# Optimization experiments

Measured on AMD Instinct MI355X. Metric: run time of the kernel, lower is better.

The kernel has to match this reference:

```python
import jax, jax.numpy as jnp
import numpy as np

H = 51  # hidden size hardcoded in the module
B, T, FUT = 4096, 512, 16


def setup_inputs() -> dict:
    key = jax.random.key(0)
    ks = jax.random.split(key, 12)
    s = 1.0 / np.sqrt(H)  # PyTorch default uniform init bound
    u = lambda k, shape: jax.random.uniform(k, shape, jnp.float32, -s, s)
    return {
        "input": jax.random.normal(ks[0], (B, T), jnp.float32),
        "W_ih1": u(ks[1], (4 * H, 1)),
        "W_hh1": u(ks[2], (4 * H, H)),
        "b_ih1": u(ks[3], (4 * H,)),
        "b_hh1": u(ks[4], (4 * H,)),
        "W_ih2": u(ks[5], (4 * H, H)),
        "W_hh2": u(ks[6], (4 * H, H)),
        "b_ih2": u(ks[7], (4 * H,)),
        "b_hh2": u(ks[8], (4 * H,)),
        "W_lin": u(ks[9], (1, H)),
        "b_lin": u(ks[10], (1,)),
        "future": FUT,
    }


def _cell(x, h, c, Wih, Whh, b):
    # PyTorch LSTMCell gate order: i, f, g, o
    g = x @ Wih.T + h @ Whh.T + b
    i, f, gg, o = jnp.split(g, 4, axis=-1)
    c = jax.nn.sigmoid(f) * c + jax.nn.sigmoid(i) * jnp.tanh(gg)
    h = jax.nn.sigmoid(o) * jnp.tanh(c)
    return h, c


def _forward(input, W_ih1, W_hh1, b_ih1, b_hh1, W_ih2, W_hh2, b_ih2, b_hh2, W_lin, b_lin, future):
    bsz = input.shape[0]
    dt = input.dtype
    b1 = b_ih1 + b_hh1
    b2 = b_ih2 + b_hh2
    z = jnp.zeros((bsz, H), dt)
    init = (z, z, z, z)

    def step(carry, x_t):
        h1, c1, h2, c2 = carry
        h1, c1 = _cell(x_t[:, None], h1, c1, W_ih1, W_hh1, b1)
        h2, c2 = _cell(h1, h2, c2, W_ih2, W_hh2, b2)
        out = h2 @ W_lin.T + b_lin  # [b, 1]
        return (h1, c1, h2, c2), out

    (h1, c1, h2, c2), outs = jax.lax.scan(step, init, input.T)  # outs: [t, b, 1]

    def fstep(carry, _):
        h1, c1, h2, c2, out = carry
        h1, c1 = _cell(out, h1, c1, W_ih1, W_hh1, b1)
        h2, c2 = _cell(h1, h2, c2, W_ih2, W_hh2, b2)
        out = h2 @ W_lin.T + b_lin
        return (h1, c1, h2, c2, out), out

    _, fouts = jax.lax.scan(fstep, (h1, c1, h2, c2, outs[-1]), None, length=future)
    all_outs = jnp.concatenate([outs, fouts], axis=0)  # [t+future, b, 1]
    return all_outs[..., 0].T  # [b, t+future]


def reference(input, W_ih1, W_hh1, b_ih1, b_hh1, W_ih2, W_hh2, b_ih2, b_hh2, W_lin, b_lin, future):
    return _forward(input, W_ih1, W_hh1, b_ih1, b_hh1, W_ih2, W_hh2, b_ih2, b_hh2, W_lin, b_lin, future)
```

## Files before the change

kernel.cpp:

```cpp
#include <hip/hip_runtime.h>

#define TSEQ 512
#define FUT  16
#define OT   (TSEQ + FUT)
#define NB   16
#define NWAVE 13
#define NTHREADS (NWAVE * 64)
#define OBS  20

typedef _Float16 f16x8 __attribute__((ext_vector_type(8)));
typedef float    f32x4 __attribute__((ext_vector_type(4)));

#define NL2E  (-1.44269504089f)
#define N2L2E (-2.88539008178f)

__device__ __forceinline__ f32x4 mfma16(f16x8 a, f16x8 b, f32x4 c) {
    return __builtin_amdgcn_mfma_f32_16x16x32_f16(a, b, c, 0, 0, 0);
}

__device__ __forceinline__ float exp2fast(float x) {
#if __has_builtin(__builtin_amdgcn_exp2f)
    return __builtin_amdgcn_exp2f(x);
#else
    float r;
    asm("v_exp_f32 %0, %1\n\ts_nop 1" : "=v"(r) : "v"(x));
    return r;
#endif
}

__device__ __forceinline__ float cell2(const f32x4 acc, float& c) {
    const float Ei = exp2fast(acc[0]);
    const float Ef = exp2fast(acc[1]);
    const float Eg = exp2fast(acc[2]);
    const float Eo = exp2fast(acc[3]);
    const float sf   = __builtin_amdgcn_rcpf(1.0f + Ef);
    const float sitg = (1.0f - Eg) * __builtin_amdgcn_rcpf((1.0f + Ei) * (1.0f + Eg));
    c = fmaf(sf, c, sitg);
    const float Ec = exp2fast(c * N2L2E);
    return (1.0f - Ec) * __builtin_amdgcn_rcpf((1.0f + Eo) * (1.0f + Ec));
}

__global__ __launch_bounds__(NTHREADS, 1) void lstm_mfma_kernel(
    const float* __restrict__ input,
    const float* __restrict__ W_ih1,
    const float* __restrict__ W_hh1,
    const float* __restrict__ b_ih1,
    const float* __restrict__ b_hh1,
    const float* __restrict__ W_ih2,
    const float* __restrict__ W_hh2,
    const float* __restrict__ b_ih2,
    const float* __restrict__ b_hh2,
    const float* __restrict__ W_lin,
    const float* __restrict__ b_lin,
    float* __restrict__ out)
{
    const int tid  = threadIdx.x;
    const int w    = tid >> 6;
    const int lane = tid & 63;
    const int n    = lane & 15;
    const int q    = lane >> 4;
    const int b0   = blockIdx.x * NB;

    __shared__ _Float16 H1[2][2][64][8] __attribute__((aligned(16)));
    __shared__ _Float16 H2[2][2][64][8] __attribute__((aligned(16)));
    __shared__ float OB[2][16][OBS] __attribute__((aligned(16)));

    const int ru  = 4 * w + (n >> 2);
    const bool rv = (ru < 51);
    const int R   = 51 * (n & 3) + (rv ? ru : 50);
    const bool olin_row = (w == 12) && (n == 12);
    const float rsc = ((n & 3) == 2) ? N2L2E : NL2E;

    f16x8 W1h[2], W1l[2], W2h[4], W2l[4];
#pragma unroll
    for (int s = 0; s < 2; ++s) {
#pragma unroll
        for (int e = 0; e < 8; ++e) {
            const int k = 32 * s + 8 * q + e;
            float wv = 0.0f;
            if (rv) {
                if (k < 51)       wv = rsc * W_hh1[R * 51 + k];
                else if (k == 51) wv = rsc * W_ih1[R];
            }
            const _Float16 hi = (_Float16)wv;
            W1h[s][e] = hi;
            W1l[s][e] = (_Float16)(wv - (float)hi);
        }
    }
#pragma unroll
    for (int s = 0; s < 4; ++s) {
#pragma unroll
        for (int e = 0; e < 8; ++e) {
            const int k = 32 * s + 8 * q + e;
            float wv = 0.0f;
            if (rv) {
                if (k < 51)                  wv = rsc * W_ih2[R * 51 + k];
                else if (k >= 64 && k < 115) wv = rsc * W_hh2[R * 51 + (k - 64)];
            } else if (olin_row) {
                if (k >= 64 && k < 115)      wv = W_lin[k - 64];
            }
            const _Float16 hi = (_Float16)wv;
            W2h[s][e] = hi;
            W2l[s][e] = (_Float16)(wv - (float)hi);
        }
    }

    const int uu = 4 * w + q;
    const bool ustore = (uu < 51);
    const bool oduty = (w == 12) && (q == 3);
    f32x4 bias1v, bias2v;
#pragma unroll
    for (int r = 0; r < 4; ++r) {
        const int row = 51 * r + (ustore ? uu : 50);
        const float s = (r == 2) ? N2L2E : NL2E;
        bias1v[r] = ustore ? s * (b_ih1[row] + b_hh1[row]) : 0.0f;
        bias2v[r] = ustore ? s * (b_ih2[row] + b_hh2[row]) : 0.0f;
    }
    const float blin = b_lin[0];
    if (oduty) bias2v[0] = blin;
    const float wlin = ustore ? W_lin[uu] : 0.0f;
    const int uuX = ustore ? uu : 60;
    const int us = uuX >> 5;
    const int lp = n + 16 * ((uuX & 31) >> 3);
    const int ue = uuX & 7;

    {
        const f16x8 zz = {0, 0, 0, 0, 0, 0, 0, 0};
        f16x8* p1 = (f16x8*)&H1[0][0][0][0];
        f16x8* p2 = (f16x8*)&H2[0][0][0][0];
        for (int i = tid; i < 2 * 2 * 64; i += NTHREADS) { p1[i] = zz; p2[i] = zz; }
    }
    __syncthreads();

    float c1 = 0.0f, c2 = 0.0f;

    f32x4 xv = {0, 0, 0, 0}, xvn = {0, 0, 0, 0};
    if (q == 2) xv = *(const f32x4*)&input[(b0 + n) * TSEQ + 0];

    f32x4 obuf = {0, 0, 0, 0};

    {
        f16x8 xk1 = {0,0,0,0,0,0,0,0}, xlo = {0,0,0,0,0,0,0,0};
        if (q == 2) {
            const _Float16 hi = (_Float16)xv[0];
            xk1[3] = hi;
            xlo[3] = (_Float16)(xv[0] - (float)hi);
        }
        f32x4 a1 = mfma16(W1h[1], xk1, bias1v);
        a1 = mfma16(W1l[1], xk1, a1);
        a1 = mfma16(W1h[1], xlo, a1);
        const float h1n = cell2(a1, c1);
        H1[1][us][lp][ue] = (_Float16)h1n;
    }
    __syncthreads();

#define PHASE(t_, R_, OSL_, OSTORE_, FLUSH_, LOADN_)                           \
    {                                                                          \
        const int p_  = (R_) & 1;                                              \
        const int pn_ = p_ ^ 1;                                                \
        if ((R_) == 0) xv = xvn;                                               \
        const f16x8 h1k0 = *(const f16x8*)&H1[p_][0][lane][0];                 \
        f16x8 h1k1       = *(const f16x8*)&H1[p_][1][lane][0];                 \
        const f16x8 h2k0 = *(const f16x8*)&H2[p_][0][lane][0];                 \
        const f16x8 h2k1 = *(const f16x8*)&H2[p_][1][lane][0];                 \
        if ((LOADN_) && q == 2)                                                \
            xvn = *(const f32x4*)&input[(b0 + n) * TSEQ + (t_) + 1];           \
        f16x8 xlo = {0,0,0,0,0,0,0,0};                                         \
        if (q == 2) {                                                          \
            const _Float16 hi = (_Float16)xv[R_];                              \
            h1k1[3] = hi;                                                      \
            xlo[3]  = (_Float16)(xv[R_] - (float)hi);                          \
        }                                                                      \
        f32x4 a1 = mfma16(W1h[0], h1k0, bias1v);                               \
        a1 = mfma16(W1l[0], h1k0, a1);                                         \
        a1 = mfma16(W1h[1], h1k1, a1);                                         \
        a1 = mfma16(W1l[1], h1k1, a1);                                         \
        a1 = mfma16(W1h[1], xlo,  a1);                                         \
        f32x4 a2 = mfma16(W2h[0], h1k0, bias2v);                               \
        a2 = mfma16(W2l[0], h1k0, a2);                                         \
        a2 = mfma16(W2h[1], h1k1, a2);                                         \
        a2 = mfma16(W2l[1], h1k1, a2);                                         \
        a2 = mfma16(W2h[2], h2k0, a2);                                         \
        a2 = mfma16(W2l[2], h2k0, a2);                                         \
        a2 = mfma16(W2h[3], h2k1, a2);                                         \
        a2 = mfma16(W2l[3], h2k1, a2);                                         \
        if (OSTORE_) obuf[OSL_] = a2[0];                                       \
        if ((FLUSH_) && oduty)                                                 \
            *reinterpret_cast<f32x4*>(&out[(b0 + n) * OT + (t_) - 5]) = obuf;  \
        const float h1n = cell2(a1, c1);                                       \
        const float h2n = cell2(a2, c2);                                       \
        H1[pn_][us][lp][ue] = (_Float16)h1n;                                   \
        H2[pn_][us][lp][ue] = (_Float16)h2n;                                   \
        __syncthreads();                                                       \
    }

    PHASE(1, 1, 0, 0, 0, 0)
    for (int tb = 2; tb + 3 < TSEQ; tb += 4) {
        PHASE(tb + 0, 2, 0, 1, 0, 0)
        PHASE(tb + 1, 3, 1, 1, 0, 1)
        PHASE(tb + 2, 0, 2, 1, 0, 0)
        PHASE(tb + 3, 1, 3, 1, 1, 0)
    }
    PHASE(510, 2, 0, 1, 0, 0)
    PHASE(511, 3, 1, 1, 0, 0)
#undef PHASE

    if (oduty) {
        out[(b0 + n) * OT + 508] = obuf[0];
        out[(b0 + n) * OT + 509] = obuf[1];
    }

    for (int t = TSEQ; t < OT; ++t) {
        const int p  = t & 1;
        const int pn = p ^ 1;

        const f16x8 h1k0 = *(const f16x8*)&H1[p][0][lane][0];
        f16x8 h1k1       = *(const f16x8*)&H1[p][1][lane][0];
        const f16x8 h2k0 = *(const f16x8*)&H2[p][0][lane][0];
        const f16x8 h2k1 = *(const f16x8*)&H2[p][1][lane][0];
        f32x4 a2 = mfma16(W2h[0], h1k0, bias2v);
        a2 = mfma16(W2l[0], h1k0, a2);
        a2 = mfma16(W2h[1], h1k1, a2);
        a2 = mfma16(W2l[1], h1k1, a2);
        a2 = mfma16(W2h[2], h2k0, a2);
        a2 = mfma16(W2l[2], h2k0, a2);
        a2 = mfma16(W2h[3], h2k1, a2);
        a2 = mfma16(W2l[3], h2k1, a2);
        if (oduty && t == TSEQ) out[(b0 + n) * OT + (TSEQ - 2)] = a2[0];
        const float h2n = cell2(a2, c2);
        H2[pn][us][lp][ue] = (_Float16)h2n;
        float po = h2n * wlin;
        po += __shfl_xor(po, 16, 64);
        po += __shfl_xor(po, 32, 64);
        if (lane < 16) OB[p][lane][w] = po;
        __syncthreads();

        float xcur = 0.0f;
        if (q == 2) {
            const float* ob = &OB[p][n][0];
            const f32x4 s0 = *(const f32x4*)&ob[0];
            const f32x4 s1 = *(const f32x4*)&ob[4];
            const f32x4 s2 = *(const f32x4*)&ob[8];
            const float o = ((s0[0] + s0[1]) + (s0[2] + s0[3]))
                          + ((s1[0] + s1[1]) + (s1[2] + s1[3]))
                          + ((s2[0] + s2[1]) + (s2[2] + s2[3])) + ob[12] + blin;
            if (w == 0) out[(b0 + n) * OT + (t - 1)] = o;
            xcur = o;
        }
        f16x8 xlo = {0,0,0,0,0,0,0,0};
        if (q == 2) {
            const _Float16 hi = (_Float16)xcur;
            h1k1[3] = hi;
            xlo[3]  = (_Float16)(xcur - (float)hi);
        }
        f32x4 a1 = mfma16(W1h[0], h1k0, bias1v);
        a1 = mfma16(W1l[0], h1k0, a1);
        a1 = mfma16(W1h[1], h1k1, a1);
        a1 = mfma16(W1l[1], h1k1, a1);
        a1 = mfma16(W1h[1], xlo,  a1);
        const float h1n = cell2(a1, c1);
        H1[pn][us][lp][ue] = (_Float16)h1n;
        __syncthreads();
    }

    {
        const f16x8 h1k0 = *(const f16x8*)&H1[0][0][lane][0];
        const f16x8 h1k1 = *(const f16x8*)&H1[0][1][lane][0];
        const f16x8 h2k0 = *(const f16x8*)&H2[0][0][lane][0];
        const f16x8 h2k1 = *(const f16x8*)&H2[0][1][lane][0];
        f32x4 a2 = mfma16(W2h[0], h1k0, bias2v);
        a2 = mfma16(W2l[0], h1k0, a2);
        a2 = mfma16(W2h[1], h1k1, a2);
        a2 = mfma16(W2l[1], h1k1, a2);
        a2 = mfma16(W2h[2], h2k0, a2);
        a2 = mfma16(W2l[2], h2k0, a2);
        a2 = mfma16(W2h[3], h2k1, a2);
        a2 = mfma16(W2l[3], h2k1, a2);
        const float h2n = cell2(a2, c2);
        float po = h2n * wlin;
        po += __shfl_xor(po, 16, 64);
        po += __shfl_xor(po, 32, 64);
        if (lane < 16) OB[0][lane][w] = po;
        __syncthreads();
        if (w == 0 && lane < 16) {
            const float* ob = &OB[0][lane][0];
            const f32x4 s0 = *(const f32x4*)&ob[0];
            const f32x4 s1 = *(const f32x4*)&ob[4];
            const f32x4 s2 = *(const f32x4*)&ob[8];
            out[(b0 + lane) * OT + (OT - 1)] =
                ((s0[0] + s0[1]) + (s0[2] + s0[3])) +
                ((s1[0] + s1[1]) + (s1[2] + s1[3])) +
                ((s2[0] + s2[1]) + (s2[2] + s2[3])) + ob[12] + blin;
        }
    }
}

extern "C" void kernel_launch(void* const* d_in, const int* in_sizes, int n_in,
                              void* d_out, int out_size, void* d_ws, size_t ws_size,
                              hipStream_t stream) {
    const float* input = (const float*)d_in[0];
    const float* W_ih1 = (const float*)d_in[1];
    const float* W_hh1 = (const float*)d_in[2];
    const float* b_ih1 = (const float*)d_in[3];
    const float* b_hh1 = (const float*)d_in[4];
    const float* W_ih2 = (const float*)d_in[5];
    const float* W_hh2 = (const float*)d_in[6];
    const float* b_ih2 = (const float*)d_in[7];
    const float* b_hh2 = (const float*)d_in[8];
    const float* W_lin = (const float*)d_in[9];
    const float* b_lin = (const float*)d_in[10];

    const int bsz = in_sizes[0] / TSEQ;

    hipLaunchKernelGGL(lstm_mfma_kernel, dim3(bsz / NB), dim3(NTHREADS), 0, stream,
                       input, W_ih1, W_hh1, b_ih1, b_hh1,
                       W_ih2, W_hh2, b_ih2, b_hh2, W_lin, b_lin,
                       (float*)d_out);
}
```

Before: 426.1 us.

## Drop fp16 input split correction and stage x_t into shared H1 by one wave

Removes the low-part correction MFMA on the scalar input (x now rounded to fp16 only), cutting one MFMA per layer-1 step. The input is now loaded and written into the shared H1 buffer slot by wave 12 one step ahead, rather than every wave patching its own register copy. This cuts per-step MFMA work and per-wave global loads on the serial critical path. In exchange it loses input precision, since x is no longer split into hi and lo fp16 parts, and it depends on the slot written into H1 lining up correctly with the double-buffer schedule.

```diff
diff --git a/kernel.cpp b/kernel.cpp
--- a/kernel.cpp
+++ b/kernel.cpp
@@ -135,47 +135,48 @@
     float c1 = 0.0f, c2 = 0.0f;
 
     f32x4 xv = {0, 0, 0, 0}, xvn = {0, 0, 0, 0};
-    if (q == 2) xv = *(const f32x4*)&input[(b0 + n) * TSEQ + 0];
+    if (w == 12 && q == 2) {
+        xv  = *(const f32x4*)&input[(b0 + n) * TSEQ + 0];
+        xvn = *(const f32x4*)&input[(b0 + n) * TSEQ + 4];
+    }
 
     f32x4 obuf = {0, 0, 0, 0};
 
     {
-        f16x8 xk1 = {0,0,0,0,0,0,0,0}, xlo = {0,0,0,0,0,0,0,0};
-        if (q == 2) {
-            const _Float16 hi = (_Float16)xv[0];
-            xk1[3] = hi;
-            xlo[3] = (_Float16)(xv[0] - (float)hi);
-        }
-        f32x4 a1 = mfma16(W1h[1], xk1, bias1v);
-        a1 = mfma16(W1l[1], xk1, a1);
-        a1 = mfma16(W1h[1], xlo, a1);
+        f16x8 xk1 = {0,0,0,0,0,0,0,0};
+        if (w == 12 && q == 2) {
+            xk1[3] = (_Float16)xv[0];
+            H1[1][1][32 + n][3] = (_Float16)xv[1];
+        }
+        float x0 = input[(b0 + n) * TSEQ + 0];
+        f16x8 xf = {0,0,0,0,0,0,0,0};
+        if (q == 2) xf[3] = (_Float16)x0;
+        f32x4 a1 = mfma16(W1h[1], xf, bias1v);
+        a1 = mfma16(W1l[1], xf, a1);
         const float h1n = cell2(a1, c1);
         H1[1][us][lp][ue] = (_Float16)h1n;
     }
     __syncthreads();
 
-#define PHASE(t_, R_, OSL_, OSTORE_, FLUSH_, LOADN_)                           \
+#define PHASE(t_, W_, ROT_, OSL_, OSTORE_, FLUSH_, LOADN_, XW_)                \
     {                                                                          \
-        const int p_  = (R_) & 1;                                              \
+        const int p_  = (t_) & 1;                                              \
         const int pn_ = p_ ^ 1;                                                \
-        if ((R_) == 0) xv = xvn;                                               \
         const f16x8 h1k0 = *(const f16x8*)&H1[p_][0][lane][0];                 \
-        f16x8 h1k1       = *(const f16x8*)&H1[p_][1][lane][0];                 \
+        const f16x8 h1k1 = *(const f16x8*)&H1[p_][1][lane][0];                 \
         const f16x8 h2k0 = *(const f16x8*)&H2[p_][0][lane][0];                 \
         const f16x8 h2k1 = *(const f16x8*)&H2[p_][1][lane][0];                 \
-        if ((LOADN_) && q == 2)                                                \
-            xvn = *(const f32x4*)&input[(b0 + n) * TSEQ + (t_) + 1];           \
-        f16x8 xlo = {0,0,0,0,0,0,0,0};                                         \
-        if (q == 2) {                                                          \
-            const _Float16 hi = (_Float16)xv[R_];                              \
-            h1k1[3] = hi;                                                      \
-            xlo[3]  = (_Float16)(xv[R_] - (float)hi);                          \
+        if (w == 12) {                                                         \
+            if (ROT_) xv = xvn;                                                \
+            if ((LOADN_) && q == 2)                                            \
+                xvn = *(const f32x4*)&input[(b0 + n) * TSEQ + (t_) + 3];       \
+            if ((XW_) && q == 2)                                               \
+                H1[pn_][1][32 + n][3] = (_Float16)xv[W_];                      \
         }                                                                      \
         f32x4 a1 = mfma16(W1h[0], h1k0, bias1v);                               \
         a1 = mfma16(W1l[0], h1k0, a1);                                         \
         a1 = mfma16(W1h[1], h1k1, a1);                                         \
         a1 = mfma16(W1l[1], h1k1, a1);                                         \
-        a1 = mfma16(W1h[1], xlo,  a1);                                         \
         f32x4 a2 = mfma16(W2h[0], h1k0, bias2v);                               \
         a2 = mfma16(W2l[0], h1k0, a2);                                         \
         a2 = mfma16(W2h[1], h1k1, a2);                                         \
@@ -194,15 +195,19 @@
         __syncthreads();                                                       \
     }
 
-    PHASE(1, 1, 0, 0, 0, 0)
-    for (int tb = 2; tb + 3 < TSEQ; tb += 4) {
-        PHASE(tb + 0, 2, 0, 1, 0, 0)
-        PHASE(tb + 1, 3, 1, 1, 0, 1)
-        PHASE(tb + 2, 0, 2, 1, 0, 0)
-        PHASE(tb + 3, 1, 3, 1, 1, 0)
-    }
-    PHASE(510, 2, 0, 1, 0, 0)
-    PHASE(511, 3, 1, 1, 0, 0)
+    PHASE(  1,   2, 0,  0,  0,  0,  0,  1)
+    for (int tb = 2; tb + 3 <= 505; tb += 4) {
+        PHASE(tb + 0, 3, 0, 0, 1, 0, 0, 1)
+        PHASE(tb + 1, 0, 1, 1, 1, 0, 0, 1)
+        PHASE(tb + 2, 1, 0, 2, 1, 0, 0, 1)
+        PHASE(tb + 3, 2, 0, 3, 1, 1, 1, 1)
+    }
+    PHASE(506, 3, 0, 0, 1, 0, 0, 1)
+    PHASE(507, 0, 1, 1, 1, 0, 0, 1)
+    PHASE(508, 1, 0, 2, 1, 0, 0, 1)
+    PHASE(509, 2, 0, 3, 1, 1, 0, 1)
+    PHASE(510, 3, 0, 0, 1, 0, 0, 1)
+    PHASE(511, 0, 0, 1, 1, 0, 0, 0)
 #undef PHASE
 
     if (oduty) {
@@ -247,17 +252,11 @@
             if (w == 0) out[(b0 + n) * OT + (t - 1)] = o;
             xcur = o;
         }
-        f16x8 xlo = {0,0,0,0,0,0,0,0};
-        if (q == 2) {
-            const _Float16 hi = (_Float16)xcur;
-            h1k1[3] = hi;
-            xlo[3]  = (_Float16)(xcur - (float)hi);
-        }
+        if (q == 2) h1k1[3] = (_Float16)xcur;
         f32x4 a1 = mfma16(W1h[0], h1k0, bias1v);
         a1 = mfma16(W1l[0], h1k0, a1);
         a1 = mfma16(W1h[1], h1k1, a1);
         a1 = mfma16(W1l[1], h1k1, a1);
-        a1 = mfma16(W1h[1], xlo,  a1);
         const float h1n = cell2(a1, c1);
         H1[pn][us][lp][ue] = (_Float16)h1n;
         __syncthreads();
```

Result: faster. 417.5 us (-2.0%).
